# Performance work log

Hardware: AMD Instinct MI355X
Metric: run time of the kernel (lower is better)

The kernel has to match this reference:

```python
import jax, jax.numpy as jnp
import numpy as np


def _bilinear_sample(img, gx, gy):
    """torch.nn.functional.grid_sample equivalent: bilinear, padding_mode='zeros',
    align_corners=True. img: [H,W]; gx,gy: normalized coords in [-1,1] (x->width, y->height)."""
    H, W = img.shape
    x = (gx + 1.0) * 0.5 * (W - 1)
    y = (gy + 1.0) * 0.5 * (H - 1)
    x0 = jnp.floor(x)
    y0 = jnp.floor(y)
    x1 = x0 + 1.0
    y1 = y0 + 1.0
    wx1 = x - x0
    wx0 = 1.0 - wx1
    wy1 = y - y0
    wy0 = 1.0 - wy1

    def gather(xi, yi):
        valid = (xi >= 0) & (xi <= W - 1) & (yi >= 0) & (yi <= H - 1)
        xc = jnp.clip(xi, 0, W - 1).astype(jnp.int32)
        yc = jnp.clip(yi, 0, H - 1).astype(jnp.int32)
        return jnp.where(valid, img[yc, xc], jnp.zeros((), img.dtype))

    return (gather(x0, y0) * wx0 * wy0 + gather(x1, y0) * wx1 * wy0 +
            gather(x0, y1) * wx0 * wy1 + gather(x1, y1) * wx1 * wy1)


def _radon_forward(img, n_angles, det_count, image_size, step_size, sampling_points):
    distance = 2.0 / image_size
    # detector shifts [D]
    sx = jnp.linspace(-1.0, 1.0, det_count) * (det_count / 2.0) * distance * step_size
    sy = -np.sqrt(2.0).astype(np.float32)
    ey = -sy
    angles = jnp.linspace(0.0, np.pi, n_angles)[:, None] + np.pi / 2.0  # [A,1]
    ca, sa = jnp.cos(angles), jnp.sin(angles)
    rsx = sx * ca - sy * sa            # [A,D] ray start x
    rsy = sx * sa + sy * ca            # [A,D] ray start y
    rdx = (sx * ca + sy * sa) - rsx    # rex - rsx  (ex=sx, ey=+sqrt2 => ex*ca - ey*sa)
    # careful: rex = ex*cos - ey*sin = sx*ca - ey*sa = sx*ca + sy*sa (since ey=-sy)
    rdy = (sx * sa - sy * ca) - rsy    # rey = ex*sin + ey*cos = sx*sa - sy*ca
    S = sampling_points
    t = (jnp.arange(S, dtype=jnp.float32) / S)[:, None, None]  # [S,1,1]
    gx = rsx[None] + t * rdx[None]     # [S,A,D]
    gy = rsy[None] + t * rdy[None]
    samples = _bilinear_sample(img, gx, gy)        # [S,A,D]
    intens = jnp.sum(samples, axis=0) / S          # [A,D]
    # torch.rot90(out, 2) on [A*D,1] then view(A,D) == flip both axes of [A,D]
    return jnp.flip(intens, (0, 1))


def setup_inputs() -> dict:
    key = jax.random.key(0)
    img = jax.random.uniform(key, (512, 512), dtype=jnp.float32)
    return {
        "input": img,
        "n_angles": 512,
        "det_count": 512,
        "image_size": 512,
        "step_size": 1,
        "sampling_points": 256,
    }


def reference(input, n_angles, det_count, image_size, step_size, sampling_points):
    return _radon_forward(input, n_angles, det_count, image_size, step_size, sampling_points)
```

## Files before the change

### kernel.cpp

```cpp
#include <hip/hip_runtime.h>
#include <math.h>

#define IMG 512
#define A_N 512
#define D_N 512
#define S_N 256
#define PAD 8
#define PW  528

struct H4 { _Float16 v00, v10, v01, v11; };

__device__ __forceinline__ float imz(const float* __restrict__ im, int y, int x) {
    return ((unsigned)y < 512u && (unsigned)x < 512u) ? im[(y << 9) + x] : 0.0f;
}

__global__ __launch_bounds__(256)
void pack_fp16(const float* __restrict__ im,
               H4* __restrict__ pack, H4* __restrict__ packT) {
    __shared__ H4 ldsT[32][33];
    const int bx = blockIdx.x % 17, by = blockIdx.x / 17;
    const int tx = threadIdx.x & 31, ty0 = threadIdx.x >> 5;
    const int p = bx * 32 + tx;
    const int x = p - PAD;
    #pragma unroll
    for (int i = 0; i < 4; ++i) {
        const int ty = ty0 + i * 8;
        const int q = by * 32 + ty;
        const int y = q - PAD;
        const float a = imz(im, y, x);
        const float b = imz(im, y, x + 1);
        const float c = imz(im, y + 1, x);
        const float d = imz(im, y + 1, x + 1);
        if (p < PW && q < PW) {
            H4 e; e.v00 = (_Float16)a; e.v10 = (_Float16)b;
                  e.v01 = (_Float16)c; e.v11 = (_Float16)d;
            pack[q * PW + p] = e;
        }
        H4 eT; eT.v00 = (_Float16)a; eT.v10 = (_Float16)c;
               eT.v01 = (_Float16)b; eT.v11 = (_Float16)d;
        ldsT[tx][ty] = eT;
    }
    __syncthreads();
    #pragma unroll
    for (int i = 0; i < 4; ++i) {
        const int r  = ty0 + i * 8;
        const int qT = bx * 32 + r;
        const int pT = by * 32 + tx;
        if (qT < PW && pT < PW)
            packT[qT * PW + pT] = ldsT[r][tx];
    }
}

struct Samp { H4 P; float fx, fy; };

__device__ __forceinline__ Samp samp_load(const H4* __restrict__ base,
                                          float Ax, float Ay,
                                          float dBx, float dBy, int s) {
    Samp r;
    const float x = fmaf((float)s, dBx, Ax);
    const float y = fmaf((float)s, dBy, Ay);
    const int ix = (int)x, iy = (int)y;
    r.P  = base[iy * PW + ix];
    r.fx = x - (float)ix;
    r.fy = y - (float)iy;
    return r;
}

__device__ __forceinline__ void samp_acc(const Samp& r, float& acc) {
    const float t_ = fmaf(r.fx, (float)r.P.v10 - (float)r.P.v00, (float)r.P.v00);
    const float b_ = fmaf(r.fx, (float)r.P.v11 - (float)r.P.v01, (float)r.P.v01);
    acc = fmaf(r.fy, b_ - t_, t_ + acc);
}

__global__ __launch_bounds__(256, 6)
void radon_fp16(const H4* __restrict__ pack, const H4* __restrict__ packT,
                float* __restrict__ out) {
    const int blk  = blockIdx.x;
    const int a    = ((blk & 7) << 6) | ((blk >> 3) & 63);
    const int dg   = (int)((0x70615243u >> ((blk >> 9) * 4)) & 7u);
    const int lane = threadIdx.x & 63;
    const int h    = threadIdx.x >> 6;
    const int d    = dg * 64 + lane;

    const float PI  = 3.14159265358979323846f;
    const float SQ2 = 1.41421356237309504880f;

    const float ang = fmaf((float)a, PI / 511.0f, PI * 0.5f);
    float sa, ca;
    sincosf(ang, &sa, &ca);

    const float sx = fmaf((float)d, 2.0f / 511.0f, -1.0f);
    float Ax = (fmaf(sx, ca,  SQ2 * sa) + 1.0f) * 255.5f;
    float Ay = (fmaf(sx, sa, -SQ2 * ca) + 1.0f) * 255.5f;
    float Bx = -2.0f * SQ2 * sa * 255.5f;
    float By =  2.0f * SQ2 * ca * 255.5f;

    const H4* base = pack;
    if (fabsf(sa) > fabsf(ca)) {
        float t;
        t = Ax; Ax = Ay; Ay = t;
        t = Bx; Bx = By; By = t;
        base = packT;
    }

    float t0 = 0.0f, t1 = 255.0f / 256.0f;
    bool ok = true;
    {
        const float ra = (-1.0f - Ax) / Bx, rb = (512.0f - Ax) / Bx;
        t0 = fmaxf(t0, fminf(ra, rb));
        t1 = fminf(t1, fmaxf(ra, rb));
    }
    if (fabsf(By) > 1e-9f) {
        const float ra = (-1.0f - Ay) / By, rb = (512.0f - Ay) / By;
        t0 = fmaxf(t0, fminf(ra, rb));
        t1 = fminf(t1, fmaxf(ra, rb));
    } else if (Ay < -1.0f || Ay > 512.0f) ok = false;

    float acc0 = 0.0f, acc1 = 0.0f, acc2 = 0.0f, acc3 = 0.0f;
    if (ok && t0 <= t1) {
        const int s0  = max(0, (int)(t0 * 256.0f) - 1);
        const int s1  = min(S_N - 1, (int)(t1 * 256.0f) + 1);
        const int len = s1 - s0 + 1;
        if (len > 0) {
            const int qn  = (len + 3) >> 2;
            const int ws0 = s0 + h * qn;
            const int ws1 = min(ws0 + qn - 1, s1);

            const float dBx = Bx * (1.0f / 256.0f);
            const float dBy = By * (1.0f / 256.0f);
            Ax += (float)PAD;
            Ay += (float)PAD;

            int s = ws0;
            const int nFull = (ws1 - ws0 + 1) >> 2;
            if (nFull > 0) {
                Samp c0 = samp_load(base, Ax, Ay, dBx, dBy, s);
                Samp c1 = samp_load(base, Ax, Ay, dBx, dBy, s + 1);
                Samp c2 = samp_load(base, Ax, Ay, dBx, dBy, s + 2);
                Samp c3 = samp_load(base, Ax, Ay, dBx, dBy, s + 3);
                for (int g = 1; g < nFull; ++g) {
                    Samp n0 = samp_load(base, Ax, Ay, dBx, dBy, s + 4);
                    Samp n1 = samp_load(base, Ax, Ay, dBx, dBy, s + 5);
                    Samp n2 = samp_load(base, Ax, Ay, dBx, dBy, s + 6);
                    Samp n3 = samp_load(base, Ax, Ay, dBx, dBy, s + 7);
                    samp_acc(c0, acc0);
                    samp_acc(c1, acc1);
                    samp_acc(c2, acc2);
                    samp_acc(c3, acc3);
                    c0 = n0; c1 = n1; c2 = n2; c3 = n3;
                    s += 4;
                }
                samp_acc(c0, acc0);
                samp_acc(c1, acc1);
                samp_acc(c2, acc2);
                samp_acc(c3, acc3);
                s += 4;
            }
            for (; s <= ws1; ++s) {
                Samp r = samp_load(base, Ax, Ay, dBx, dBy, s);
                samp_acc(r, acc0);
            }
        }
    }
    const float acc = (acc0 + acc1) + (acc2 + acc3);

    __shared__ float red[256];
    red[threadIdx.x] = acc;
    __syncthreads();
    if (threadIdx.x < 64) {
        const float v = (red[threadIdx.x] + red[threadIdx.x + 64] +
                         red[threadIdx.x + 128] + red[threadIdx.x + 192]) * (1.0f / 256.0f);
        const int dd = dg * 64 + threadIdx.x;
        out[(511 - a) * 512 + (511 - dd)] = v;
    }
}

__global__ __launch_bounds__(256)
void radon_direct(const float* __restrict__ img, float* __restrict__ out) {
    const int tid = blockIdx.x * 256 + threadIdx.x;
    const int d = tid & (D_N - 1);
    const int a = tid >> 9;
    const float PI  = 3.14159265358979323846f;
    const float SQ2 = 1.41421356237309504880f;
    const float ang = fmaf((float)a, PI / 511.0f, PI * 0.5f);
    float sa, ca;
    sincosf(ang, &sa, &ca);
    const float sx = fmaf((float)d, 2.0f / 511.0f, -1.0f);
    const float Ax = (fmaf(sx, ca,  SQ2 * sa) + 1.0f) * 255.5f;
    const float Ay = (fmaf(sx, sa, -SQ2 * ca) + 1.0f) * 255.5f;
    const float Bx = -2.0f * SQ2 * sa * 255.5f;
    const float By =  2.0f * SQ2 * ca * 255.5f;
    float acc = 0.0f;
    for (int s = 0; s < S_N; ++s) {
        const float t = (float)s * (1.0f / 256.0f);
        const float x = fmaf(t, Bx, Ax);
        const float y = fmaf(t, By, Ay);
        const float xf = floorf(x), yf = floorf(y);
        const float fx = x - xf, fy = y - yf;
        const int ix = (int)xf, iy = (int)yf;
        float wx0 = 1.0f - fx, wx1 = fx, wy0 = 1.0f - fy, wy1 = fy;
        wx0 = ((unsigned)ix       < 512u) ? wx0 : 0.0f;
        wx1 = ((unsigned)(ix + 1) < 512u) ? wx1 : 0.0f;
        wy0 = ((unsigned)iy       < 512u) ? wy0 : 0.0f;
        wy1 = ((unsigned)(iy + 1) < 512u) ? wy1 : 0.0f;
        const int ix0 = min(max(ix, 0), 511), ix1 = min(max(ix + 1, 0), 511);
        const int iy0 = min(max(iy, 0), 511), iy1 = min(max(iy + 1, 0), 511);
        const float* r0 = img + (iy0 << 9);
        const float* r1 = img + (iy1 << 9);
        acc = fmaf(fmaf(r0[ix1], wx1, r0[ix0] * wx0), wy0, acc);
        acc = fmaf(fmaf(r1[ix1], wx1, r1[ix0] * wx0), wy1, acc);
    }
    out[(511 - a) * 512 + (511 - d)] = acc * (1.0f / 256.0f);
}

extern "C" void kernel_launch(void* const* d_in, const int* in_sizes, int n_in,
                              void* d_out, int out_size, void* d_ws, size_t ws_size,
                              hipStream_t stream) {
    const float* img = (const float*)d_in[0];
    float* out = (float*)d_out;
    const size_t packBytes = (size_t)PW * PW * sizeof(H4);

    if (ws_size >= 2 * packBytes) {
        H4* pack  = (H4*)d_ws;
        H4* packT = pack + (size_t)PW * PW;
        pack_fp16<<<17 * 17, 256, 0, stream>>>(img, pack, packT);
        radon_fp16<<<4096, 256, 0, stream>>>(pack, packT, out);
    } else {
        radon_direct<<<(A_N * D_N) / 256, 256, 0, stream>>>(img, out);
    }
}
```

Measured before the change: 134.0 us.

## Store x-differences in fp16 pack and interleave sample split within wavefronts

```diff
diff --git a/kernel.cpp b/kernel.cpp
--- a/kernel.cpp
+++ b/kernel.cpp
@@ -8,7 +8,7 @@
 #define PAD 8
 #define PW  528
 
-struct H4 { _Float16 v00, v10, v01, v11; };
+struct H4 { _Float16 v00, dx0, v01, dx1; };
 
 __device__ __forceinline__ float imz(const float* __restrict__ im, int y, int x) {
     return ((unsigned)y < 512u && (unsigned)x < 512u) ? im[(y << 9) + x] : 0.0f;
@@ -32,12 +32,12 @@
         const float c = imz(im, y + 1, x);
         const float d = imz(im, y + 1, x + 1);
         if (p < PW && q < PW) {
-            H4 e; e.v00 = (_Float16)a; e.v10 = (_Float16)b;
-                  e.v01 = (_Float16)c; e.v11 = (_Float16)d;
+            H4 e; e.v00 = (_Float16)a; e.dx0 = (_Float16)(b - a);
+                  e.v01 = (_Float16)c; e.dx1 = (_Float16)(d - c);
             pack[q * PW + p] = e;
         }
-        H4 eT; eT.v00 = (_Float16)a; eT.v10 = (_Float16)c;
-               eT.v01 = (_Float16)b; eT.v11 = (_Float16)d;
+        H4 eT; eT.v00 = (_Float16)a; eT.dx0 = (_Float16)(c - a);
+               eT.v01 = (_Float16)b; eT.dx1 = (_Float16)(d - b);
         ldsT[tx][ty] = eT;
     }
     __syncthreads();
@@ -67,8 +67,8 @@
 }
 
 __device__ __forceinline__ void samp_acc(const Samp& r, float& acc) {
-    const float t_ = fmaf(r.fx, (float)r.P.v10 - (float)r.P.v00, (float)r.P.v00);
-    const float b_ = fmaf(r.fx, (float)r.P.v11 - (float)r.P.v01, (float)r.P.v01);
+    const float t_ = fmaf(r.fx, (float)r.P.dx0, (float)r.P.v00);
+    const float b_ = fmaf(r.fx, (float)r.P.dx1, (float)r.P.v01);
     acc = fmaf(r.fy, b_ - t_, t_ + acc);
 }
 
@@ -78,9 +78,11 @@
     const int blk  = blockIdx.x;
     const int a    = ((blk & 7) << 6) | ((blk >> 3) & 63);
     const int dg   = (int)((0x70615243u >> ((blk >> 9) * 4)) & 7u);
+    const int w    = threadIdx.x >> 6;
     const int lane = threadIdx.x & 63;
-    const int h    = threadIdx.x >> 6;
-    const int d    = dg * 64 + lane;
+    const int di   = lane & 15;
+    const int js   = lane >> 4;
+    const int d    = dg * 64 + w * 16 + di;
 
     const float PI  = 3.14159265358979323846f;
     const float SQ2 = 1.41421356237309504880f;
@@ -120,56 +122,56 @@
     if (ok && t0 <= t1) {
         const int s0  = max(0, (int)(t0 * 256.0f) - 1);
         const int s1  = min(S_N - 1, (int)(t1 * 256.0f) + 1);
-        const int len = s1 - s0 + 1;
-        if (len > 0) {
-            const int qn  = (len + 3) >> 2;
-            const int ws0 = s0 + h * qn;
-            const int ws1 = min(ws0 + qn - 1, s1);
-
-            const float dBx = Bx * (1.0f / 256.0f);
-            const float dBy = By * (1.0f / 256.0f);
-            Ax += (float)PAD;
-            Ay += (float)PAD;
-
-            int s = ws0;
-            const int nFull = (ws1 - ws0 + 1) >> 2;
-            if (nFull > 0) {
-                Samp c0 = samp_load(base, Ax, Ay, dBx, dBy, s);
-                Samp c1 = samp_load(base, Ax, Ay, dBx, dBy, s + 1);
-                Samp c2 = samp_load(base, Ax, Ay, dBx, dBy, s + 2);
-                Samp c3 = samp_load(base, Ax, Ay, dBx, dBy, s + 3);
-                for (int g = 1; g < nFull; ++g) {
-                    Samp n0 = samp_load(base, Ax, Ay, dBx, dBy, s + 4);
-                    Samp n1 = samp_load(base, Ax, Ay, dBx, dBy, s + 5);
-                    Samp n2 = samp_load(base, Ax, Ay, dBx, dBy, s + 6);
-                    Samp n3 = samp_load(base, Ax, Ay, dBx, dBy, s + 7);
-                    samp_acc(c0, acc0);
-                    samp_acc(c1, acc1);
-                    samp_acc(c2, acc2);
-                    samp_acc(c3, acc3);
-                    c0 = n0; c1 = n1; c2 = n2; c3 = n3;
-                    s += 4;
-                }
+        const int m   = s1 - (s0 + js);
+        const int nk  = (m >= 0) ? ((m >> 2) + 1) : 0;
+
+        const float dBx = Bx * (1.0f / 256.0f);
+        const float dBy = By * (1.0f / 256.0f);
+        Ax += (float)PAD;
+        Ay += (float)PAD;
+
+        int s = s0 + js;
+        int k = 0;
+        const int nFull = nk >> 2;
+        if (nFull > 0) {
+            Samp c0 = samp_load(base, Ax, Ay, dBx, dBy, s);
+            Samp c1 = samp_load(base, Ax, Ay, dBx, dBy, s + 4);
+            Samp c2 = samp_load(base, Ax, Ay, dBx, dBy, s + 8);
+            Samp c3 = samp_load(base, Ax, Ay, dBx, dBy, s + 12);
+            for (int g = 1; g < nFull; ++g) {
+                Samp n0 = samp_load(base, Ax, Ay, dBx, dBy, s + 16);
+                Samp n1 = samp_load(base, Ax, Ay, dBx, dBy, s + 20);
+                Samp n2 = samp_load(base, Ax, Ay, dBx, dBy, s + 24);
+                Samp n3 = samp_load(base, Ax, Ay, dBx, dBy, s + 28);
                 samp_acc(c0, acc0);
                 samp_acc(c1, acc1);
                 samp_acc(c2, acc2);
                 samp_acc(c3, acc3);
-                s += 4;
+                c0 = n0; c1 = n1; c2 = n2; c3 = n3;
+                s += 16;
             }
-            for (; s <= ws1; ++s) {
-                Samp r = samp_load(base, Ax, Ay, dBx, dBy, s);
-                samp_acc(r, acc0);
-            }
+            samp_acc(c0, acc0);
+            samp_acc(c1, acc1);
+            samp_acc(c2, acc2);
+            samp_acc(c3, acc3);
+            s += 16;
+            k = nFull << 2;
         }
-    }
-    const float acc = (acc0 + acc1) + (acc2 + acc3);
-
-    __shared__ float red[256];
-    red[threadIdx.x] = acc;
+        for (; k < nk; ++k, s += 4) {
+            Samp r = samp_load(base, Ax, Ay, dBx, dBy, s);
+            samp_acc(r, acc0);
+        }
+    }
+    float acc = (acc0 + acc1) + (acc2 + acc3);
+
+    acc += __shfl_xor(acc, 16);
+    acc += __shfl_xor(acc, 32);
+
+    __shared__ float red[64];
+    if (lane < 16) red[w * 16 + di] = acc;
     __syncthreads();
     if (threadIdx.x < 64) {
-        const float v = (red[threadIdx.x] + red[threadIdx.x + 64] +
-                         red[threadIdx.x + 128] + red[threadIdx.x + 192]) * (1.0f / 256.0f);
+        const float v = red[threadIdx.x] * (1.0f / 256.0f);
         const int dd = dg * 64 + threadIdx.x;
         out[(511 - a) * 512 + (511 - dd)] = v;
     }
```

Result: faster. 123.2 us (-8.0%).
